# Optimization experiments

Hardware: AMD Instinct MI355X
Metric: run time of the kernel (lower is better)

The kernel has to match this reference:

```python
import jax, jax.numpy as jnp
import numpy as np
import math

D_IN, D_MODEL, D_STATE, STAGES, N_CLS = 2048, 64, 128, 20, 202
PHASE_MAX = math.pi / 50


def _layer_norm(x, g, b, eps=1e-5):
    mu = jnp.mean(x, axis=-1, keepdims=True)
    var = jnp.mean((x - mu) ** 2, axis=-1, keepdims=True)
    return (x - mu) * jax.lax.rsqrt(var + eps) * g + b


def _lru_scan(z, nu_log, theta_log, gamma_log, B_re, B_im, C_re, C_im, Dskip):
    # z: (B,T,D_MODEL). Diagonal complex linear recurrence h_t = lam*h_{t-1} + gamma*(B z_t).
    lam = jnp.exp(-jnp.exp(nu_log) + 1j * jnp.exp(theta_log))          # (N,) complex, |lam|<1
    gamma = jnp.exp(gamma_log)                                          # (N,)
    u = (jnp.einsum('btd,nd->btn', z, B_re)
         + 1j * jnp.einsum('btd,nd->btn', z, B_im)) * gamma             # (B,T,N) complex
    lam_bc = jnp.broadcast_to(lam, u.shape)

    def binop(a, b):
        la, ua = a
        lb, ub = b
        return la * lb, lb * ua + ub

    _, h = jax.lax.associative_scan(binop, (lam_bc, u), axis=1)         # (B,T,N) complex
    y = (jnp.einsum('btn,dn->btd', h.real, C_re)
         - jnp.einsum('btn,dn->btd', h.imag, C_im))                     # Re(C h)
    return y + Dskip * z


def setup_inputs() -> dict:
    key = jax.random.key(0)
    ks = jax.random.split(key, 16)
    x = jax.random.normal(ks[0], (8, 2048, D_IN), dtype=jnp.float32)

    ln0_g = jnp.ones((D_IN,), jnp.float32)
    ln0_b = jnp.zeros((D_IN,), jnp.float32)
    W_embed = jax.random.normal(ks[1], (D_IN, D_MODEL), jnp.float32) / np.sqrt(D_IN)
    b_embed = jnp.zeros((D_MODEL,), jnp.float32)

    # per-stage LRU params, stacked over STAGES
    r = jax.random.uniform(ks[2], (STAGES, D_STATE), minval=0.9, maxval=0.999)
    theta = jax.random.uniform(ks[3], (STAGES, D_STATE), minval=1e-4, maxval=PHASE_MAX)
    nu_log = jnp.log(-jnp.log(r))
    theta_log = jnp.log(theta)
    gamma_log = 0.5 * jnp.log(1.0 - r ** 2)
    B_re = jax.random.normal(ks[4], (STAGES, D_STATE, D_MODEL)) / np.sqrt(2 * D_MODEL)
    B_im = jax.random.normal(ks[5], (STAGES, D_STATE, D_MODEL)) / np.sqrt(2 * D_MODEL)
    C_re = jax.random.normal(ks[6], (STAGES, D_MODEL, D_STATE)) / np.sqrt(D_STATE)
    C_im = jax.random.normal(ks[7], (STAGES, D_MODEL, D_STATE)) / np.sqrt(D_STATE)
    Dskip = jax.random.normal(ks[8], (STAGES, D_MODEL))
    ln_g = jnp.ones((STAGES, D_MODEL), jnp.float32)
    ln_b = jnp.zeros((STAGES, D_MODEL), jnp.float32)

    W_cls = jax.random.normal(ks[9], (D_MODEL, N_CLS), jnp.float32) / np.sqrt(D_MODEL)
    b_cls = jnp.zeros((N_CLS,), jnp.float32)

    return dict(x=x, ln0_g=ln0_g, ln0_b=ln0_b, W_embed=W_embed, b_embed=b_embed,
                ln_g=ln_g, ln_b=ln_b, nu_log=nu_log, theta_log=theta_log,
                gamma_log=gamma_log, B_re=B_re, B_im=B_im, C_re=C_re, C_im=C_im,
                Dskip=Dskip, W_cls=W_cls, b_cls=b_cls)


def reference(x, ln0_g, ln0_b, W_embed, b_embed, ln_g, ln_b, nu_log, theta_log,
              gamma_log, B_re, B_im, C_re, C_im, Dskip, W_cls, b_cls):
    # dropout is identity at inference
    h = _layer_norm(x, ln0_g, ln0_b)
    h = h @ W_embed + b_embed                                           # (B,T,64)
    for s in range(STAGES):
        z = _layer_norm(h, ln_g[s], ln_b[s])
        h = h + _lru_scan(z, nu_log[s], theta_log[s], gamma_log[s],
                          B_re[s], B_im[s], C_re[s], C_im[s], Dskip[s])
    out = h @ W_cls + b_cls                                             # (B,T,202)
    return out[None, ...]                                               # (1,B,T,202)
```

## Files before the change

### kernel.cpp

```cpp
#include <hip/hip_runtime.h>

typedef float f32x4 __attribute__((ext_vector_type(4)));
typedef __bf16 bf16x8 __attribute__((ext_vector_type(8)));

#define NSTAGE 20
#define TSEQ   2048
#define NST    128
#define NP2    256
#define NCLS   202
#define NCHUNK 32
#define CHTOK  64

static __device__ __forceinline__ unsigned short f2b(float f) {
  return __builtin_bit_cast(unsigned short, (__bf16)f);
}

__global__ void lru_convert_kernel(const float* __restrict__ Wemb,
                                   const float* __restrict__ Bre, const float* __restrict__ Bim,
                                   const float* __restrict__ Cre, const float* __restrict__ Cim,
                                   const float* __restrict__ Wcls,
                                   unsigned short* __restrict__ Wt,
                                   unsigned short* __restrict__ Bws,
                                   unsigned short* __restrict__ Cws,
                                   unsigned short* __restrict__ Wclst)
{
  const int NWT = 64 * 2048;
  const int NB  = NSTAGE * NP2 * 64;
  const int NC  = NSTAGE * 64 * NP2;
  const int NWC = 208 * 64;
  int idx = blockIdx.x * 256 + threadIdx.x;
  if (idx < NWT) {
    int d = idx >> 11, k = idx & 2047;
    Wt[idx] = f2b(Wemb[k * 64 + d]);
  } else if (idx < NWT + NB) {
    int r = idx - NWT;
    int s = r / (NP2 * 64); int r2 = r % (NP2 * 64);
    int np = r2 >> 6, k = r2 & 63;
    int n = np >> 1, p = np & 1;
    float v = p ? Bim[(s * NST + n) * 64 + k] : Bre[(s * NST + n) * 64 + k];
    Bws[r] = f2b(v);
  } else if (idx < NWT + NB + NC) {
    int r = idx - NWT - NB;
    int s = r / (64 * NP2); int r2 = r % (64 * NP2);
    int d = r2 >> 8, np = r2 & 255;
    int n = np >> 1, p = np & 1;
    float v = p ? -Cim[(s * 64 + d) * NST + n] : Cre[(s * 64 + d) * NST + n];
    Cws[r] = f2b(v);
  } else if (idx < NWT + NB + NC + NWC) {
    int r = idx - NWT - NB - NC;
    int cls = r >> 6, k = r & 63;
    Wclst[r] = (cls < NCLS) ? f2b(Wcls[k * NCLS + cls]) : (unsigned short)0;
  }
}

__launch_bounds__(256)
__global__ void lru_embed_kernel(const float* __restrict__ x,
                                 const float* __restrict__ g0,
                                 const float* __restrict__ b0,
                                 const unsigned short* __restrict__ Wt,
                                 const float* __restrict__ bemb,
                                 float* __restrict__ h0)
{
  __shared__ __align__(16) unsigned short zb[16][72];
  __shared__ float mu_s[16], rs_s[16];

  const int tid = threadIdx.x;
  const int b  = blockIdx.x >> 7;
  const int t0 = (blockIdx.x & 127) * 16;
  const int w = tid >> 6, lane = tid & 63;
  const int cl = lane & 15, q = lane >> 4;
  const int tg = tid >> 4, g = tid & 15;

  for (int i = 0; i < 4; ++i) {
    int t = w * 4 + i;
    const float* xp = x + ((size_t)(b * TSEQ + t0 + t)) * 2048;
    float sum = 0.f, sq = 0.f;
    #pragma unroll
    for (int j = 0; j < 32; ++j) {
      float v = xp[lane + 64 * j];
      sum += v; sq += v * v;
    }
    #pragma unroll
    for (int m = 1; m < 64; m <<= 1) {
      sum += __shfl_xor(sum, m); sq += __shfl_xor(sq, m);
    }
    if (lane == 0) {
      float mu = sum * (1.f / 2048.f);
      float var = sq * (1.f / 2048.f) - mu * mu;
      mu_s[t] = mu;
      rs_s[t] = rsqrtf(var + 1e-5f);
    }
  }
  __syncthreads();

  {
    const int g4 = g * 4;
    const float muT = mu_s[tg], rsT = rs_s[tg];
    f32x4 acc = {0.f, 0.f, 0.f, 0.f};
    for (int kc = 0; kc < 32; ++kc) {
      __syncthreads();
      {
        const float* xp = x + ((size_t)(b * TSEQ + t0 + tg)) * 2048 + kc * 64 + g4;
        float4 xv = *(const float4*)xp;
        float4 gv = *(const float4*)&g0[kc * 64 + g4];
        float4 bv = *(const float4*)&b0[kc * 64 + g4];
        float z0 = (xv.x - muT) * rsT * gv.x + bv.x;
        float z1 = (xv.y - muT) * rsT * gv.y + bv.y;
        float z2 = (xv.z - muT) * rsT * gv.z + bv.z;
        float z3 = (xv.w - muT) * rsT * gv.w + bv.w;
        *(unsigned*)&zb[tg][g4]     = (unsigned)f2b(z0) | ((unsigned)f2b(z1) << 16);
        *(unsigned*)&zb[tg][g4 + 2] = (unsigned)f2b(z2) | ((unsigned)f2b(z3) << 16);
      }
      __syncthreads();
      bf16x8 a0 = *(const bf16x8*)((const char*)&zb[0][0] + cl * 144 + q * 16);
      bf16x8 a1 = *(const bf16x8*)((const char*)&zb[0][0] + cl * 144 + 64 + q * 16);
      const unsigned short* wp = Wt + ((size_t)(w * 16 + cl)) * 2048 + kc * 64 + q * 8;
      bf16x8 w0 = *(const bf16x8*)wp;
      bf16x8 w1 = *(const bf16x8*)(wp + 32);
      acc = __builtin_amdgcn_mfma_f32_16x16x32_bf16(a0, w0, acc, 0, 0, 0);
      acc = __builtin_amdgcn_mfma_f32_16x16x32_bf16(a1, w1, acc, 0, 0, 0);
    }
    int d = w * 16 + cl;
    float be = bemb[d];
    #pragma unroll
    for (int r = 0; r < 4; ++r)
      h0[((size_t)(b * TSEQ + t0 + q * 4 + r)) * 64 + d] = acc[r] + be;
  }
}

__launch_bounds__(256)
__global__ void lru_carry0_kernel(const float* __restrict__ h0,
                                  const unsigned short* __restrict__ Bws,
                                  const float* __restrict__ lng,
                                  const float* __restrict__ lnb,
                                  const float* __restrict__ nulog,
                                  const float* __restrict__ thlog,
                                  const float* __restrict__ gmlog,
                                  float* __restrict__ carr)
{
  __shared__ __align__(16) unsigned short zb[16][72];
  __shared__ __align__(16) float ucat[16][264];

  const int tid = threadIdx.x;
  const int b = blockIdx.x >> 5;
  const int c = blockIdx.x & 31;
  const int t0 = c * CHTOK;
  const int w = tid >> 6, lane = tid & 63;
  const int cl = lane & 15, q = lane >> 4;
  const int tg = tid >> 4, g = tid & 15;

  float lamr = 0.f, lami = 0.f, hr = 0.f, hi = 0.f;
  if (tid < NST) {
    float mag = __expf(-__expf(nulog[tid]));
    float th  = __expf(thlog[tid]);
    lamr = mag * __cosf(th);
    lami = mag * __sinf(th);
  }

  for (int sb = 0; sb < 4; ++sb) {
    int tb = t0 + sb * 16;
    __syncthreads();
    {
      float4 hv = *(const float4*)&h0[((size_t)(b * TSEQ + tb + tg)) * 64 + g * 4];
      float sum = hv.x + hv.y + hv.z + hv.w;
      sum += __shfl_xor(sum, 1); sum += __shfl_xor(sum, 2);
      sum += __shfl_xor(sum, 4); sum += __shfl_xor(sum, 8);
      float mu = sum * (1.f / 64.f);
      float d0 = hv.x - mu, d1 = hv.y - mu, d2 = hv.z - mu, d3 = hv.w - mu;
      float sq = d0 * d0 + d1 * d1 + d2 * d2 + d3 * d3;
      sq += __shfl_xor(sq, 1); sq += __shfl_xor(sq, 2);
      sq += __shfl_xor(sq, 4); sq += __shfl_xor(sq, 8);
      float rs = rsqrtf(sq * (1.f / 64.f) + 1e-5f);
      float4 gv = *(const float4*)&lng[g * 4];
      float4 bv = *(const float4*)&lnb[g * 4];
      float z0 = d0 * rs * gv.x + bv.x;
      float z1 = d1 * rs * gv.y + bv.y;
      float z2 = d2 * rs * gv.z + bv.z;
      float z3 = d3 * rs * gv.w + bv.w;
      *(unsigned*)&zb[tg][g * 4]     = (unsigned)f2b(z0) | ((unsigned)f2b(z1) << 16);
      *(unsigned*)&zb[tg][g * 4 + 2] = (unsigned)f2b(z2) | ((unsigned)f2b(z3) << 16);
    }
    __syncthreads();
    {
      bf16x8 a0 = *(const bf16x8*)((const char*)&zb[0][0] + cl * 144 + q * 16);
      bf16x8 a1 = *(const bf16x8*)((const char*)&zb[0][0] + cl * 144 + 64 + q * 16);
      #pragma unroll
      for (int ti = 0; ti < 4; ++ti) {
        int np0 = (w * 4 + ti) * 16;
        const unsigned short* bp = Bws + (np0 + cl) * 64 + q * 8;
        bf16x8 b0 = *(const bf16x8*)bp;
        bf16x8 b1 = *(const bf16x8*)(bp + 32);
        f32x4 acc = {0.f, 0.f, 0.f, 0.f};
        acc = __builtin_amdgcn_mfma_f32_16x16x32_bf16(a0, b0, acc, 0, 0, 0);
        acc = __builtin_amdgcn_mfma_f32_16x16x32_bf16(a1, b1, acc, 0, 0, 0);
        int np = np0 + cl;
        float gam = __expf(gmlog[np >> 1]);
        ucat[q * 4 + 0][np] = acc[0] * gam;
        ucat[q * 4 + 1][np] = acc[1] * gam;
        ucat[q * 4 + 2][np] = acc[2] * gam;
        ucat[q * 4 + 3][np] = acc[3] * gam;
      }
    }
    __syncthreads();
    if (tid < NST) {
      int n = tid;
      #pragma unroll
      for (int t = 0; t < 16; ++t) {
        float ur = ucat[t][2 * n], ui = ucat[t][2 * n + 1];
        float nr = fmaf(lamr, hr, fmaf(-lami, hi, ur));
        float ni = fmaf(lamr, hi, fmaf(lami, hr, ui));
        hr = nr; hi = ni;
      }
    }
  }
  if (tid < NST) {
    float* cw = carr + ((size_t)(b * NCHUNK + c)) * 256 + 2 * tid;
    cw[0] = hr;
    cw[1] = hi;
  }
}

__launch_bounds__(256)
__global__ void lru_applycarry_kernel(float* __restrict__ h0,
                                      const float* __restrict__ carrin,
                                      float* __restrict__ carrout,
                                      const unsigned short* __restrict__ Bws,
                                      const unsigned short* __restrict__ Cws,
                                      const float* __restrict__ lng,
                                      const float* __restrict__ lnb,
                                      const float* __restrict__ nulog,
                                      const float* __restrict__ thlog,
                                      const float* __restrict__ gmlog,
                                      const float* __restrict__ dskip,
                                      int s, int last,
                                      const unsigned short* __restrict__ Wclst,
                                      const float* __restrict__ bcls,
                                      float* __restrict__ out)
{
  __shared__ float hsm64[64][68];
  __shared__ float hs[16][68];
  __shared__ float zsm[16][68];
  __shared__ __align__(16) unsigned short zb[16][72];
  __shared__ __align__(16) float ucat[16][264];
  __shared__ __align__(16) unsigned short hcb[16][264];

  const int tid = threadIdx.x;
  const int b = blockIdx.x >> 5;
  const int c = blockIdx.x & 31;
  const int t0 = c * CHTOK;
  const int w = tid >> 6, lane = tid & 63;
  const int cl = lane & 15, q = lane >> 4;
  const int tg = tid >> 4, g = tid & 15;

  float lamr = 0.f, lami = 0.f, Pr = 0.f, Pi = 0.f;
  if (tid < NST) {
    int n = tid;
    float mag = __expf(-__expf(nulog[s * NST + n]));
    float th  = __expf(thlog[s * NST + n]);
    lamr = mag * __cosf(th);
    lami = mag * __sinf(th);
    float ar = lamr, ai = lami;
    #pragma unroll
    for (int it = 0; it < 6; ++it) {
      float nr = ar * ar - ai * ai;
      float ni = 2.f * ar * ai;
      ar = nr; ai = ni;
    }
    const float* cb = carrin + (size_t)b * NCHUNK * 256 + 2 * n;
    #pragma unroll 4
    for (int j = 0; j < c; ++j) {
      float cr = cb[j * 256];
      float ci = cb[j * 256 + 1];
      float nr = fmaf(ar, Pr, fmaf(-ai, Pi, cr));
      float ni = fmaf(ar, Pi, fmaf(ai, Pr, ci));
      Pr = nr; Pi = ni;
    }
  }

  float hr = Pr, hi = Pi;
  for (int sb = 0; sb < 4; ++sb) {
    int tb = t0 + sb * 16;
    __syncthreads();
    {
      float4 hv = *(const float4*)&h0[((size_t)(b * TSEQ + tb + tg)) * 64 + g * 4];
      hs[tg][g * 4 + 0] = hv.x; hs[tg][g * 4 + 1] = hv.y;
      hs[tg][g * 4 + 2] = hv.z; hs[tg][g * 4 + 3] = hv.w;
      float sum = hv.x + hv.y + hv.z + hv.w;
      sum += __shfl_xor(sum, 1); sum += __shfl_xor(sum, 2);
      sum += __shfl_xor(sum, 4); sum += __shfl_xor(sum, 8);
      float mu = sum * (1.f / 64.f);
      float d0 = hv.x - mu, d1 = hv.y - mu, d2 = hv.z - mu, d3 = hv.w - mu;
      float sq = d0 * d0 + d1 * d1 + d2 * d2 + d3 * d3;
      sq += __shfl_xor(sq, 1); sq += __shfl_xor(sq, 2);
      sq += __shfl_xor(sq, 4); sq += __shfl_xor(sq, 8);
      float rs = rsqrtf(sq * (1.f / 64.f) + 1e-5f);
      float4 gv = *(const float4*)&lng[s * 64 + g * 4];
      float4 bv = *(const float4*)&lnb[s * 64 + g * 4];
      float z0 = d0 * rs * gv.x + bv.x;
      float z1 = d1 * rs * gv.y + bv.y;
      float z2 = d2 * rs * gv.z + bv.z;
      float z3 = d3 * rs * gv.w + bv.w;
      zsm[tg][g * 4 + 0] = z0; zsm[tg][g * 4 + 1] = z1;
      zsm[tg][g * 4 + 2] = z2; zsm[tg][g * 4 + 3] = z3;
      *(unsigned*)&zb[tg][g * 4]     = (unsigned)f2b(z0) | ((unsigned)f2b(z1) << 16);
      *(unsigned*)&zb[tg][g * 4 + 2] = (unsigned)f2b(z2) | ((unsigned)f2b(z3) << 16);
    }
    __syncthreads();
    {
      bf16x8 a0 = *(const bf16x8*)((const char*)&zb[0][0] + cl * 144 + q * 16);
      bf16x8 a1 = *(const bf16x8*)((const char*)&zb[0][0] + cl * 144 + 64 + q * 16);
      const unsigned short* bb = Bws + (size_t)s * NP2 * 64;
      #pragma unroll
      for (int ti = 0; ti < 4; ++ti) {
        int np0 = (w * 4 + ti) * 16;
        const unsigned short* bp = bb + (np0 + cl) * 64 + q * 8;
        bf16x8 b0 = *(const bf16x8*)bp;
        bf16x8 b1 = *(const bf16x8*)(bp + 32);
        f32x4 acc = {0.f, 0.f, 0.f, 0.f};
        acc = __builtin_amdgcn_mfma_f32_16x16x32_bf16(a0, b0, acc, 0, 0, 0);
        acc = __builtin_amdgcn_mfma_f32_16x16x32_bf16(a1, b1, acc, 0, 0, 0);
        int np = np0 + cl;
        float gam = __expf(gmlog[s * NST + (np >> 1)]);
        ucat[q * 4 + 0][np] = acc[0] * gam;
        ucat[q * 4 + 1][np] = acc[1] * gam;
        ucat[q * 4 + 2][np] = acc[2] * gam;
        ucat[q * 4 + 3][np] = acc[3] * gam;
      }
    }
    __syncthreads();
    if (tid < NST) {
      int n = tid;
      #pragma unroll
      for (int t = 0; t < 16; ++t) {
        float ur = ucat[t][2 * n], ui = ucat[t][2 * n + 1];
        float nr = fmaf(lamr, hr, fmaf(-lami, hi, ur));
        float ni = fmaf(lamr, hi, fmaf(lami, hr, ui));
        hr = nr; hi = ni;
        *(unsigned*)&hcb[t][2 * n] = (unsigned)f2b(hr) | ((unsigned)f2b(hi) << 16);
      }
    }
    __syncthreads();
    {
      int d0 = w * 16;
      const unsigned short* cp = Cws + ((size_t)s * 64 + d0 + cl) * NP2 + q * 8;
      f32x4 acc = {0.f, 0.f, 0.f, 0.f};
      #pragma unroll
      for (int ks = 0; ks < 8; ++ks) {
        bf16x8 a  = *(const bf16x8*)((const char*)&hcb[0][0] + cl * 528 + ks * 64 + q * 16);
        bf16x8 cc = *(const bf16x8*)(cp + ks * 32);
        acc = __builtin_amdgcn_mfma_f32_16x16x32_bf16(a, cc, acc, 0, 0, 0);
      }
      int d = d0 + cl;
      float dk = dskip[s * 64 + d];
      #pragma unroll
      for (int r = 0; r < 4; ++r) {
        int t = q * 4 + r;
        hsm64[sb * 16 + t][d] = hs[t][d] + acc[r] + dk * zsm[t][d];
      }
    }
  }

  if (!last) {
    const int s1 = s + 1;
    float lam2r = 0.f, lam2i = 0.f, h2r = 0.f, h2i = 0.f;
    if (tid < NST) {
      float mag = __expf(-__expf(nulog[s1 * NST + tid]));
      float th  = __expf(thlog[s1 * NST + tid]);
      lam2r = mag * __cosf(th);
      lam2i = mag * __sinf(th);
    }
    for (int sb = 0; sb < 4; ++sb) {
      __syncthreads();
      {
        float4 hv = *(const float4*)&hsm64[sb * 16 + tg][g * 4];
        float sum = hv.x + hv.y + hv.z + hv.w;
        sum += __shfl_xor(sum, 1); sum += __shfl_xor(sum, 2);
        sum += __shfl_xor(sum, 4); sum += __shfl_xor(sum, 8);
        float mu = sum * (1.f / 64.f);
        float d0 = hv.x - mu, d1 = hv.y - mu, d2 = hv.z - mu, d3 = hv.w - mu;
        float sq = d0 * d0 + d1 * d1 + d2 * d2 + d3 * d3;
        sq += __shfl_xor(sq, 1); sq += __shfl_xor(sq, 2);
        sq += __shfl_xor(sq, 4); sq += __shfl_xor(sq, 8);
        float rs = rsqrtf(sq * (1.f / 64.f) + 1e-5f);
        float4 gv = *(const float4*)&lng[s1 * 64 + g * 4];
        float4 bv = *(const float4*)&lnb[s1 * 64 + g * 4];
        float z0 = d0 * rs * gv.x + bv.x;
        float z1 = d1 * rs * gv.y + bv.y;
        float z2 = d2 * rs * gv.z + bv.z;
        float z3 = d3 * rs * gv.w + bv.w;
        *(unsigned*)&zb[tg][g * 4]     = (unsigned)f2b(z0) | ((unsigned)f2b(z1) << 16);
        *(unsigned*)&zb[tg][g * 4 + 2] = (unsigned)f2b(z2) | ((unsigned)f2b(z3) << 16);
      }
      __syncthreads();
      {
        bf16x8 a0 = *(const bf16x8*)((const char*)&zb[0][0] + cl * 144 + q * 16);
        bf16x8 a1 = *(const bf16x8*)((const char*)&zb[0][0] + cl * 144 + 64 + q * 16);
        const unsigned short* bb = Bws + (size_t)s1 * NP2 * 64;
        #pragma unroll
        for (int ti = 0; ti < 4; ++ti) {
          int np0 = (w * 4 + ti) * 16;
          const unsigned short* bp = bb + (np0 + cl) * 64 + q * 8;
          bf16x8 b0 = *(const bf16x8*)bp;
          bf16x8 b1 = *(const bf16x8*)(bp + 32);
          f32x4 acc = {0.f, 0.f, 0.f, 0.f};
          acc = __builtin_amdgcn_mfma_f32_16x16x32_bf16(a0, b0, acc, 0, 0, 0);
          acc = __builtin_amdgcn_mfma_f32_16x16x32_bf16(a1, b1, acc, 0, 0, 0);
          int np = np0 + cl;
          float gam = __expf(gmlog[s1 * NST + (np >> 1)]);
          ucat[q * 4 + 0][np] = acc[0] * gam;
          ucat[q * 4 + 1][np] = acc[1] * gam;
          ucat[q * 4 + 2][np] = acc[2] * gam;
          ucat[q * 4 + 3][np] = acc[3] * gam;
        }
      }
      __syncthreads();
      if (tid < NST) {
        int n = tid;
        #pragma unroll
        for (int t = 0; t < 16; ++t) {
          float ur = ucat[t][2 * n], ui = ucat[t][2 * n + 1];
          float nr = fmaf(lam2r, h2r, fmaf(-lam2i, h2i, ur));
          float ni = fmaf(lam2r, h2i, fmaf(lam2i, h2r, ui));
          h2r = nr; h2i = ni;
        }
      }
    }
    if (tid < NST) {
      float* cw = carrout + ((size_t)(b * NCHUNK + c)) * 256 + 2 * tid;
      cw[0] = h2r;
      cw[1] = h2i;
    }
    #pragma unroll
    for (int sb = 0; sb < 4; ++sb) {
      float4 hv;
      hv.x = hsm64[sb * 16 + tg][g * 4 + 0];
      hv.y = hsm64[sb * 16 + tg][g * 4 + 1];
      hv.z = hsm64[sb * 16 + tg][g * 4 + 2];
      hv.w = hsm64[sb * 16 + tg][g * 4 + 3];
      *(float4*)&h0[((size_t)(b * TSEQ + t0 + sb * 16 + tg)) * 64 + g * 4] = hv;
    }
  } else {
    for (int sb = 0; sb < 4; ++sb) {
      int tb = t0 + sb * 16;
      __syncthreads();
      {
        *(unsigned*)&zb[tg][g * 4] =
            (unsigned)f2b(hsm64[sb * 16 + tg][g * 4 + 0]) |
            ((unsigned)f2b(hsm64[sb * 16 + tg][g * 4 + 1]) << 16);
        *(unsigned*)&zb[tg][g * 4 + 2] =
            (unsigned)f2b(hsm64[sb * 16 + tg][g * 4 + 2]) |
            ((unsigned)f2b(hsm64[sb * 16 + tg][g * 4 + 3]) << 16);
      }
      __syncthreads();
      bf16x8 a0 = *(const bf16x8*)((const char*)&zb[0][0] + cl * 144 + q * 16);
      bf16x8 a1 = *(const bf16x8*)((const char*)&zb[0][0] + cl * 144 + 64 + q * 16);
      for (int ti = w; ti < 13; ti += 4) {
        int cls0 = ti * 16;
        const unsigned short* wp = Wclst + (cls0 + cl) * 64 + q * 8;
        bf16x8 b0 = *(const bf16x8*)wp;
        bf16x8 b1 = *(const bf16x8*)(wp + 32);
        f32x4 acc = {0.f, 0.f, 0.f, 0.f};
        acc = __builtin_amdgcn_mfma_f32_16x16x32_bf16(a0, b0, acc, 0, 0, 0);
        acc = __builtin_amdgcn_mfma_f32_16x16x32_bf16(a1, b1, acc, 0, 0, 0);
        int cls = cls0 + cl;
        if (cls < NCLS) {
          float bc = bcls[cls];
          #pragma unroll
          for (int r = 0; r < 4; ++r) {
            int t = q * 4 + r;
            out[((size_t)(b * TSEQ + tb + t)) * NCLS + cls] = acc[r] + bc;
          }
        }
      }
    }
  }
}

extern "C" void kernel_launch(void* const* d_in, const int* in_sizes, int n_in,
                              void* d_out, int out_size, void* d_ws, size_t ws_size,
                              hipStream_t stream) {
  (void)in_sizes; (void)n_in; (void)out_size; (void)ws_size;
  const float* x     = (const float*)d_in[0];
  const float* ln0g  = (const float*)d_in[1];
  const float* ln0b  = (const float*)d_in[2];
  const float* Wemb  = (const float*)d_in[3];
  const float* bemb  = (const float*)d_in[4];
  const float* lng   = (const float*)d_in[5];
  const float* lnb   = (const float*)d_in[6];
  const float* nulog = (const float*)d_in[7];
  const float* thlog = (const float*)d_in[8];
  const float* gmlog = (const float*)d_in[9];
  const float* Bre   = (const float*)d_in[10];
  const float* Bim   = (const float*)d_in[11];
  const float* Cre   = (const float*)d_in[12];
  const float* Cim   = (const float*)d_in[13];
  const float* dskip = (const float*)d_in[14];
  const float* Wcls  = (const float*)d_in[15];
  const float* bcls  = (const float*)d_in[16];
  float* out = (float*)d_out;

  char* ws = (char*)d_ws;
  float* carrA         = (float*)(ws + 0);
  float* carrB         = (float*)(ws + 262144);
  unsigned short* Bws  = (unsigned short*)(ws + 524288);
  unsigned short* Cws  = (unsigned short*)(ws + 1179648);
  unsigned short* Wt   = (unsigned short*)(ws + 1835008);
  unsigned short* Wcl  = (unsigned short*)(ws + 2097152);
  float* h0            = (float*)(ws + 2123776);

  lru_convert_kernel<<<3124, 256, 0, stream>>>(Wemb, Bre, Bim, Cre, Cim, Wcls,
                                               Wt, Bws, Cws, Wcl);
  lru_embed_kernel<<<1024, 256, 0, stream>>>(x, ln0g, ln0b, Wt, bemb, h0);
  lru_carry0_kernel<<<256, 256, 0, stream>>>(h0, Bws, lng, lnb,
                                             nulog, thlog, gmlog, carrA);
  for (int s = 0; s < NSTAGE; ++s) {
    float* cin  = (s & 1) ? carrB : carrA;
    float* cout = (s & 1) ? carrA : carrB;
    lru_applycarry_kernel<<<256, 256, 0, stream>>>(h0, cin, cout, Bws, Cws,
                                                   lng, lnb, nulog, thlog,
                                                   gmlog, dskip, s,
                                                   (s == NSTAGE - 1) ? 1 : 0,
                                                   Wcl, bcls, out);
  }
}
```

Measured before the change: 661.2 us.

## Shrink scan chunks to 16 tokens, fuse carry0 into embed, drop LDS staging

The chunked scan now uses 128 chunks of 16 tokens per batch instead of 32 chunks of 64. Each stage kernel therefore launches 1024 blocks rather than 256 and processes a single 16-token tile with no inner sub-block loop. The first-stage carry computation is fused into the embed kernel, removing one launch and a reread of h0. The embed GEMM now builds MFMA operands directly in registers, dropping the shared-memory staging and barriers. The cost is a longer serial carry-prefix loop per block (up to 127 carries instead of 31) and a four-times larger carry buffer.

Measured after the change: 856.7 us. 1.3x slower.

```diff
diff --git a/kernel.cpp b/kernel.cpp
--- a/kernel.cpp
+++ b/kernel.cpp
@@ -8,8 +8,6 @@
 #define NST    128
 #define NP2    256
 #define NCLS   202
-#define NCHUNK 32
-#define CHTOK  64
 
 static __device__ __forceinline__ unsigned short f2b(float f) {
   return __builtin_bit_cast(unsigned short, (__bf16)f);
@@ -59,14 +57,24 @@
                                  const float* __restrict__ b0,
                                  const unsigned short* __restrict__ Wt,
                                  const float* __restrict__ bemb,
-                                 float* __restrict__ h0)
+                                 const unsigned short* __restrict__ Bws,
+                                 const float* __restrict__ lng,
+                                 const float* __restrict__ lnb,
+                                 const float* __restrict__ nulog,
+                                 const float* __restrict__ thlog,
+                                 const float* __restrict__ gmlog,
+                                 float* __restrict__ h0,
+                                 float* __restrict__ carr)
 {
+  __shared__ float mu_s[16], rs_s[16];
+  __shared__ float hs[16][68];
   __shared__ __align__(16) unsigned short zb[16][72];
-  __shared__ float mu_s[16], rs_s[16];
+  __shared__ __align__(16) float ucat[16][264];
 
   const int tid = threadIdx.x;
   const int b  = blockIdx.x >> 7;
-  const int t0 = (blockIdx.x & 127) * 16;
+  const int c  = blockIdx.x & 127;
+  const int t0 = c * 16;
   const int w = tid >> 6, lane = tid & 63;
   const int cl = lane & 15, q = lane >> 4;
   const int tg = tid >> 4, g = tid & 15;
@@ -94,127 +102,108 @@
   __syncthreads();
 
   {
-    const int g4 = g * 4;
-    const float muT = mu_s[tg], rsT = rs_s[tg];
+    const float muT = mu_s[cl], rsT = rs_s[cl];
+    const float* xrow = x + ((size_t)(b * TSEQ + t0 + cl)) * 2048;
+    const unsigned short* wrow = Wt + ((size_t)(w * 16 + cl)) * 2048;
     f32x4 acc = {0.f, 0.f, 0.f, 0.f};
     for (int kc = 0; kc < 32; ++kc) {
-      __syncthreads();
-      {
-        const float* xp = x + ((size_t)(b * TSEQ + t0 + tg)) * 2048 + kc * 64 + g4;
-        float4 xv = *(const float4*)xp;
-        float4 gv = *(const float4*)&g0[kc * 64 + g4];
-        float4 bv = *(const float4*)&b0[kc * 64 + g4];
-        float z0 = (xv.x - muT) * rsT * gv.x + bv.x;
-        float z1 = (xv.y - muT) * rsT * gv.y + bv.y;
-        float z2 = (xv.z - muT) * rsT * gv.z + bv.z;
-        float z3 = (xv.w - muT) * rsT * gv.w + bv.w;
-        *(unsigned*)&zb[tg][g4]     = (unsigned)f2b(z0) | ((unsigned)f2b(z1) << 16);
-        *(unsigned*)&zb[tg][g4 + 2] = (unsigned)f2b(z2) | ((unsigned)f2b(z3) << 16);
+      #pragma unroll
+      for (int ks = 0; ks < 2; ++ks) {
+        int ko = kc * 64 + ks * 32 + q * 8;
+        float4 xa = *(const float4*)&xrow[ko];
+        float4 xb = *(const float4*)&xrow[ko + 4];
+        float4 ga = *(const float4*)&g0[ko];
+        float4 gb = *(const float4*)&g0[ko + 4];
+        float4 ba = *(const float4*)&b0[ko];
+        float4 bb = *(const float4*)&b0[ko + 4];
+        float z0 = (xa.x - muT) * rsT * ga.x + ba.x;
+        float z1 = (xa.y - muT) * rsT * ga.y + ba.y;
+        float z2 = (xa.z - muT) * rsT * ga.z + ba.z;
+        float z3 = (xa.w - muT) * rsT * ga.w + ba.w;
+        float z4 = (xb.x - muT) * rsT * gb.x + bb.x;
+        float z5 = (xb.y - muT) * rsT * gb.y + bb.y;
+        float z6 = (xb.z - muT) * rsT * gb.z + bb.z;
+        float z7 = (xb.w - muT) * rsT * gb.w + bb.w;
+        uint4 u;
+        u.x = (unsigned)f2b(z0) | ((unsigned)f2b(z1) << 16);
+        u.y = (unsigned)f2b(z2) | ((unsigned)f2b(z3) << 16);
+        u.z = (unsigned)f2b(z4) | ((unsigned)f2b(z5) << 16);
+        u.w = (unsigned)f2b(z6) | ((unsigned)f2b(z7) << 16);
+        bf16x8 a = __builtin_bit_cast(bf16x8, u);
+        bf16x8 wv = *(const bf16x8*)&wrow[ko];
+        acc = __builtin_amdgcn_mfma_f32_16x16x32_bf16(a, wv, acc, 0, 0, 0);
       }
-      __syncthreads();
-      bf16x8 a0 = *(const bf16x8*)((const char*)&zb[0][0] + cl * 144 + q * 16);
-      bf16x8 a1 = *(const bf16x8*)((const char*)&zb[0][0] + cl * 144 + 64 + q * 16);
-      const unsigned short* wp = Wt + ((size_t)(w * 16 + cl)) * 2048 + kc * 64 + q * 8;
-      bf16x8 w0 = *(const bf16x8*)wp;
-      bf16x8 w1 = *(const bf16x8*)(wp + 32);
-      acc = __builtin_amdgcn_mfma_f32_16x16x32_bf16(a0, w0, acc, 0, 0, 0);
-      acc = __builtin_amdgcn_mfma_f32_16x16x32_bf16(a1, w1, acc, 0, 0, 0);
     }
     int d = w * 16 + cl;
     float be = bemb[d];
     #pragma unroll
-    for (int r = 0; r < 4; ++r)
-      h0[((size_t)(b * TSEQ + t0 + q * 4 + r)) * 64 + d] = acc[r] + be;
-  }
-}
-
-__launch_bounds__(256)
-__global__ void lru_carry0_kernel(const float* __restrict__ h0,
-                                  const unsigned short* __restrict__ Bws,
-                                  const float* __restrict__ lng,
-                                  const float* __restrict__ lnb,
-                                  const float* __restrict__ nulog,
-                                  const float* __restrict__ thlog,
-                                  const float* __restrict__ gmlog,
-                                  float* __restrict__ carr)
-{
-  __shared__ __align__(16) unsigned short zb[16][72];
-  __shared__ __align__(16) float ucat[16][264];
-
-  const int tid = threadIdx.x;
-  const int b = blockIdx.x >> 5;
-  const int c = blockIdx.x & 31;
-  const int t0 = c * CHTOK;
-  const int w = tid >> 6, lane = tid & 63;
-  const int cl = lane & 15, q = lane >> 4;
-  const int tg = tid >> 4, g = tid & 15;
-
-  float lamr = 0.f, lami = 0.f, hr = 0.f, hi = 0.f;
+    for (int r = 0; r < 4; ++r) {
+      float hv = acc[r] + be;
+      hs[q * 4 + r][d] = hv;
+      h0[((size_t)(b * TSEQ + t0 + q * 4 + r)) * 64 + d] = hv;
+    }
+  }
+  __syncthreads();
+
+  {
+    float4 hv = *(const float4*)&hs[tg][g * 4];
+    float sum = hv.x + hv.y + hv.z + hv.w;
+    sum += __shfl_xor(sum, 1); sum += __shfl_xor(sum, 2);
+    sum += __shfl_xor(sum, 4); sum += __shfl_xor(sum, 8);
+    float mu = sum * (1.f / 64.f);
+    float d0 = hv.x - mu, d1 = hv.y - mu, d2 = hv.z - mu, d3 = hv.w - mu;
+    float sq = d0 * d0 + d1 * d1 + d2 * d2 + d3 * d3;
+    sq += __shfl_xor(sq, 1); sq += __shfl_xor(sq, 2);
+    sq += __shfl_xor(sq, 4); sq += __shfl_xor(sq, 8);
+    float rs = rsqrtf(sq * (1.f / 64.f) + 1e-5f);
+    float4 gv = *(const float4*)&lng[g * 4];
+    float4 bv = *(const float4*)&lnb[g * 4];
+    float z0 = d0 * rs * gv.x + bv.x;
+    float z1 = d1 * rs * gv.y + bv.y;
+    float z2 = d2 * rs * gv.z + bv.z;
+    float z3 = d3 * rs * gv.w + bv.w;
+    *(unsigned*)&zb[tg][g * 4]     = (unsigned)f2b(z0) | ((unsigned)f2b(z1) << 16);
+    *(unsigned*)&zb[tg][g * 4 + 2] = (unsigned)f2b(z2) | ((unsigned)f2b(z3) << 16);
+  }
+  __syncthreads();
+
+  {
+    bf16x8 a0 = *(const bf16x8*)((const char*)&zb[0][0] + cl * 144 + q * 16);
+    bf16x8 a1 = *(const bf16x8*)((const char*)&zb[0][0] + cl * 144 + 64 + q * 16);
+    #pragma unroll
+    for (int ti = 0; ti < 4; ++ti) {
+      int np0 = (w * 4 + ti) * 16;
+      const unsigned short* bp = Bws + (np0 + cl) * 64 + q * 8;
+      bf16x8 b0v = *(const bf16x8*)bp;
+      bf16x8 b1v = *(const bf16x8*)(bp + 32);
+      f32x4 acc = {0.f, 0.f, 0.f, 0.f};
+      acc = __builtin_amdgcn_mfma_f32_16x16x32_bf16(a0, b0v, acc, 0, 0, 0);
+      acc = __builtin_amdgcn_mfma_f32_16x16x32_bf16(a1, b1v, acc, 0, 0, 0);
+      int np = np0 + cl;
+      float gam = __expf(gmlog[np >> 1]);
+      ucat[q * 4 + 0][np] = acc[0] * gam;
+      ucat[q * 4 + 1][np] = acc[1] * gam;
+      ucat[q * 4 + 2][np] = acc[2] * gam;
+      ucat[q * 4 + 3][np] = acc[3] * gam;
+    }
+  }
+  __syncthreads();
+
   if (tid < NST) {
-    float mag = __expf(-__expf(nulog[tid]));
-    float th  = __expf(thlog[tid]);
-    lamr = mag * __cosf(th);
-    lami = mag * __sinf(th);
-  }
-
-  for (int sb = 0; sb < 4; ++sb) {
-    int tb = t0 + sb * 16;
-    __syncthreads();
-    {
-      float4 hv = *(const float4*)&h0[((size_t)(b * TSEQ + tb + tg)) * 64 + g * 4];
-      float sum = hv.x + hv.y + hv.z + hv.w;
-      sum += __shfl_xor(sum, 1); sum += __shfl_xor(sum, 2);
-      sum += __shfl_xor(sum, 4); sum += __shfl_xor(sum, 8);
-      float mu = sum * (1.f / 64.f);
-      float d0 = hv.x - mu, d1 = hv.y - mu, d2 = hv.z - mu, d3 = hv.w - mu;
-      float sq = d0 * d0 + d1 * d1 + d2 * d2 + d3 * d3;
-      sq += __shfl_xor(sq, 1); sq += __shfl_xor(sq, 2);
-      sq += __shfl_xor(sq, 4); sq += __shfl_xor(sq, 8);
-      float rs = rsqrtf(sq * (1.f / 64.f) + 1e-5f);
-      float4 gv = *(const float4*)&lng[g * 4];
-      float4 bv = *(const float4*)&lnb[g * 4];
-      float z0 = d0 * rs * gv.x + bv.x;
-      float z1 = d1 * rs * gv.y + bv.y;
-      float z2 = d2 * rs * gv.z + bv.z;
-      float z3 = d3 * rs * gv.w + bv.w;
-      *(unsigned*)&zb[tg][g * 4]     = (unsigned)f2b(z0) | ((unsigned)f2b(z1) << 16);
-      *(unsigned*)&zb[tg][g * 4 + 2] = (unsigned)f2b(z2) | ((unsigned)f2b(z3) << 16);
-    }
-    __syncthreads();
-    {
-      bf16x8 a0 = *(const bf16x8*)((const char*)&zb[0][0] + cl * 144 + q * 16);
-      bf16x8 a1 = *(const bf16x8*)((const char*)&zb[0][0] + cl * 144 + 64 + q * 16);
-      #pragma unroll
-      for (int ti = 0; ti < 4; ++ti) {
-        int np0 = (w * 4 + ti) * 16;
-        const unsigned short* bp = Bws + (np0 + cl) * 64 + q * 8;
-        bf16x8 b0 = *(const bf16x8*)bp;
-        bf16x8 b1 = *(const bf16x8*)(bp + 32);
-        f32x4 acc = {0.f, 0.f, 0.f, 0.f};
-        acc = __builtin_amdgcn_mfma_f32_16x16x32_bf16(a0, b0, acc, 0, 0, 0);
-        acc = __builtin_amdgcn_mfma_f32_16x16x32_bf16(a1, b1, acc, 0, 0, 0);
-        int np = np0 + cl;
-        float gam = __expf(gmlog[np >> 1]);
-        ucat[q * 4 + 0][np] = acc[0] * gam;
-        ucat[q * 4 + 1][np] = acc[1] * gam;
-        ucat[q * 4 + 2][np] = acc[2] * gam;
-        ucat[q * 4 + 3][np] = acc[3] * gam;
-      }
-    }
-    __syncthreads();
-    if (tid < NST) {
-      int n = tid;
-      #pragma unroll
-      for (int t = 0; t < 16; ++t) {
-        float ur = ucat[t][2 * n], ui = ucat[t][2 * n + 1];
-        float nr = fmaf(lamr, hr, fmaf(-lami, hi, ur));
-        float ni = fmaf(lamr, hi, fmaf(lami, hr, ui));
-        hr = nr; hi = ni;
-      }
-    }
-  }
-  if (tid < NST) {
-    float* cw = carr + ((size_t)(b * NCHUNK + c)) * 256 + 2 * tid;
+    int n = tid;
+    float mag = __expf(-__expf(nulog[n]));
+    float th  = __expf(thlog[n]);
+    float lamr = mag * __cosf(th);
+    float lami = mag * __sinf(th);
+    float hr = 0.f, hi = 0.f;
+    #pragma unroll
+    for (int t = 0; t < 16; ++t) {
+      float ur = ucat[t][2 * n], ui = ucat[t][2 * n + 1];
+      float nr = fmaf(lamr, hr, fmaf(-lami, hi, ur));
+      float ni = fmaf(lamr, hi, fmaf(lami, hr, ui));
+      hr = nr; hi = ni;
+    }
+    float* cw = carr + ((size_t)(b * 128 + c)) * 256 + 2 * n;
     cw[0] = hr;
     cw[1] = hi;
   }
@@ -237,7 +226,6 @@
                                       const float* __restrict__ bcls,
                                       float* __restrict__ out)
 {
-  __shared__ float hsm64[64][68];
   __shared__ float hs[16][68];
   __shared__ float zsm[16][68];
   __shared__ __align__(16) unsigned short zb[16][72];
@@ -245,9 +233,9 @@
   __shared__ __align__(16) unsigned short hcb[16][264];
 
   const int tid = threadIdx.x;
-  const int b = blockIdx.x >> 5;
-  const int c = blockIdx.x & 31;
-  const int t0 = c * CHTOK;
+  const int b = blockIdx.x >> 7;
+  const int c = blockIdx.x & 127;
+  const int t0 = c * 16;
   const int w = tid >> 6, lane = tid & 63;
   const int cl = lane & 15, q = lane >> 4;
   const int tg = tid >> 4, g = tid & 15;
@@ -261,12 +249,12 @@
     lami = mag * __sinf(th);
     float ar = lamr, ai = lami;
     #pragma unroll
-    for (int it = 0; it < 6; ++it) {
+    for (int it = 0; it < 4; ++it) {
       float nr = ar * ar - ai * ai;
       float ni = 2.f * ar * ai;
       ar = nr; ai = ni;
     }
-    const float* cb = carrin + (size_t)b * NCHUNK * 256 + 2 * n;
+    const float* cb = carrin + (size_t)b * 128 * 256 + 2 * n;
     #pragma unroll 4
     for (int j = 0; j < c; ++j) {
       float cr = cb[j * 256];
@@ -277,14 +265,93 @@
     }
   }
 
-  float hr = Pr, hi = Pi;
-  for (int sb = 0; sb < 4; ++sb) {
-    int tb = t0 + sb * 16;
-    __syncthreads();
+  {
+    float4 hv = *(const float4*)&h0[((size_t)(b * TSEQ + t0 + tg)) * 64 + g * 4];
+    hs[tg][g * 4 + 0] = hv.x; hs[tg][g * 4 + 1] = hv.y;
+    hs[tg][g * 4 + 2] = hv.z; hs[tg][g * 4 + 3] = hv.w;
+    float sum = hv.x + hv.y + hv.z + hv.w;
+    sum += __shfl_xor(sum, 1); sum += __shfl_xor(sum, 2);
+    sum += __shfl_xor(sum, 4); sum += __shfl_xor(sum, 8);
+    float mu = sum * (1.f / 64.f);
+    float d0 = hv.x - mu, d1 = hv.y - mu, d2 = hv.z - mu, d3 = hv.w - mu;
+    float sq = d0 * d0 + d1 * d1 + d2 * d2 + d3 * d3;
+    sq += __shfl_xor(sq, 1); sq += __shfl_xor(sq, 2);
+    sq += __shfl_xor(sq, 4); sq += __shfl_xor(sq, 8);
+    float rs = rsqrtf(sq * (1.f / 64.f) + 1e-5f);
+    float4 gv = *(const float4*)&lng[s * 64 + g * 4];
+    float4 bv = *(const float4*)&lnb[s * 64 + g * 4];
+    float z0 = d0 * rs * gv.x + bv.x;
+    float z1 = d1 * rs * gv.y + bv.y;
+    float z2 = d2 * rs * gv.z + bv.z;
+    float z3 = d3 * rs * gv.w + bv.w;
+    zsm[tg][g * 4 + 0] = z0; zsm[tg][g * 4 + 1] = z1;
+    zsm[tg][g * 4 + 2] = z2; zsm[tg][g * 4 + 3] = z3;
+    *(unsigned*)&zb[tg][g * 4]     = (unsigned)f2b(z0) | ((unsigned)f2b(z1) << 16);
+    *(unsigned*)&zb[tg][g * 4 + 2] = (unsigned)f2b(z2) | ((unsigned)f2b(z3) << 16);
+  }
+  __syncthreads();
+
+  {
+    bf16x8 a0 = *(const bf16x8*)((const char*)&zb[0][0] + cl * 144 + q * 16);
+    bf16x8 a1 = *(const bf16x8*)((const char*)&zb[0][0] + cl * 144 + 64 + q * 16);
+    const unsigned short* bb = Bws + (size_t)s * NP2 * 64;
+    #pragma unroll
+    for (int ti = 0; ti < 4; ++ti) {
+      int np0 = (w * 4 + ti) * 16;
+      const unsigned short* bp = bb + (np0 + cl) * 64 + q * 8;
+      bf16x8 b0v = *(const bf16x8*)bp;
+      bf16x8 b1v = *(const bf16x8*)(bp + 32);
+      f32x4 acc = {0.f, 0.f, 0.f, 0.f};
+      acc = __builtin_amdgcn_mfma_f32_16x16x32_bf16(a0, b0v, acc, 0, 0, 0);
+      acc = __builtin_amdgcn_mfma_f32_16x16x32_bf16(a1, b1v, acc, 0, 0, 0);
+      int np = np0 + cl;
+      float gam = __expf(gmlog[s * NST + (np >> 1)]);
+      ucat[q * 4 + 0][np] = acc[0] * gam;
+      ucat[q * 4 + 1][np] = acc[1] * gam;
+      ucat[q * 4 + 2][np] = acc[2] * gam;
+      ucat[q * 4 + 3][np] = acc[3] * gam;
+    }
+  }
+  __syncthreads();
+
+  if (tid < NST) {
+    int n = tid;
+    float hr = Pr, hi = Pi;
+    #pragma unroll
+    for (int t = 0; t < 16; ++t) {
+      float ur = ucat[t][2 * n], ui = ucat[t][2 * n + 1];
+      float nr = fmaf(lamr, hr, fmaf(-lami, hi, ur));
+      float ni = fmaf(lamr, hi, fmaf(lami, hr, ui));
+      hr = nr; hi = ni;
+      *(unsigned*)&hcb[t][2 * n] = (unsigned)f2b(hr) | ((unsigned)f2b(hi) << 16);
+    }
+  }
+  __syncthreads();
+
+  {
+    int d0 = w * 16;
+    const unsigned short* cp = Cws + ((size_t)s * 64 + d0 + cl) * NP2 + q * 8;
+    f32x4 acc = {0.f, 0.f, 0.f, 0.f};
+    #pragma unroll
+    for (int ks = 0; ks < 8; ++ks) {
+      bf16x8 a  = *(const bf16x8*)((const char*)&hcb[0][0] + cl * 528 + ks * 64 + q * 16);
+      bf16x8 cc = *(const bf16x8*)(cp + ks * 32);
+      acc = __builtin_amdgcn_mfma_f32_16x16x32_bf16(a, cc, acc, 0, 0, 0);
+    }
+    int d = d0 + cl;
+    float dk = dskip[s * 64 + d];
+    #pragma unroll
+    for (int r = 0; r < 4; ++r) {
+      int t = q * 4 + r;
+      hs[t][d] = hs[t][d] + acc[r] + dk * zsm[t][d];
+    }
+  }
+  __syncthreads();
+
+  if (!last) {
+    const int s1 = s + 1;
     {
-      float4 hv = *(const float4*)&h0[((size_t)(b * TSEQ + tb + tg)) * 64 + g * 4];
-      hs[tg][g * 4 + 0] = hv.x; hs[tg][g * 4 + 1] = hv.y;
-      hs[tg][g * 4 + 2] = hv.z; hs[tg][g * 4 + 3] = hv.w;
+      float4 hv = *(const float4*)&hs[tg][g * 4];
       float sum = hv.x + hv.y + hv.z + hv.w;
       sum += __shfl_xor(sum, 1); sum += __shfl_xor(sum, 2);
       sum += __shfl_xor(sum, 4); sum += __shfl_xor(sum, 8);
@@ -294,14 +361,12 @@
       sq += __shfl_xor(sq, 1); sq += __shfl_xor(sq, 2);
       sq += __shfl_xor(sq, 4); sq += __shfl_xor(sq, 8);
       float rs = rsqrtf(sq * (1.f / 64.f) + 1e-5f);
-      float4 gv = *(const float4*)&lng[s * 64 + g * 4];
-      float4 bv = *(const float4*)&lnb[s * 64 + g * 4];
+      float4 gv = *(const float4*)&lng[s1 * 64 + g * 4];
+      float4 bv = *(const float4*)&lnb[s1 * 64 + g * 4];
       float z0 = d0 * rs * gv.x + bv.x;
       float z1 = d1 * rs * gv.y + bv.y;
       float z2 = d2 * rs * gv.z + bv.z;
       float z3 = d3 * rs * gv.w + bv.w;
-      zsm[tg][g * 4 + 0] = z0; zsm[tg][g * 4 + 1] = z1;
-      zsm[tg][g * 4 + 2] = z2; zsm[tg][g * 4 + 3] = z3;
       *(unsigned*)&zb[tg][g * 4]     = (unsigned)f2b(z0) | ((unsigned)f2b(z1) << 16);
       *(unsigned*)&zb[tg][g * 4 + 2] = (unsigned)f2b(z2) | ((unsigned)f2b(z3) << 16);
     }
@@ -309,18 +374,18 @@
     {
       bf16x8 a0 = *(const bf16x8*)((const char*)&zb[0][0] + cl * 144 + q * 16);
       bf16x8 a1 = *(const bf16x8*)((const char*)&zb[0][0] + cl * 144 + 64 + q * 16);
-      const unsigned short* bb = Bws + (size_t)s * NP2 * 64;
+      const unsigned short* bb = Bws + (size_t)s1 * NP2 * 64;
       #pragma unroll
       for (int ti = 0; ti < 4; ++ti) {
         int np0 = (w * 4 + ti) * 16;
         const unsigned short* bp = bb + (np0 + cl) * 64 + q * 8;
-        bf16x8 b0 = *(const bf16x8*)bp;
-        bf16x8 b1 = *(const bf16x8*)(bp + 32);
+        bf16x8 b0v = *(const bf16x8*)bp;
+        bf16x8 b1v = *(const bf16x8*)(bp + 32);
         f32x4 acc = {0.f, 0.f, 0.f, 0.f};
-        acc = __builtin_amdgcn_mfma_f32_16x16x32_bf16(a0, b0, acc, 0, 0, 0);
-        acc = __builtin_amdgcn_mfma_f32_16x16x32_bf16(a1, b1, acc, 0, 0, 0);
+        acc = __builtin_amdgcn_mfma_f32_16x16x32_bf16(a0, b0v, acc, 0, 0, 0);
+        acc = __builtin_amdgcn_mfma_f32_16x16x32_bf16(a1, b1v, acc, 0, 0, 0);
         int np = np0 + cl;
-        float gam = __expf(gmlog[s * NST + (np >> 1)]);
+        float gam = __expf(gmlog[s1 * NST + (np >> 1)]);
         ucat[q * 4 + 0][np] = acc[0] * gam;
         ucat[q * 4 + 1][np] = acc[1] * gam;
         ucat[q * 4 + 2][np] = acc[2] * gam;
@@ -330,146 +395,53 @@
     __syncthreads();
     if (tid < NST) {
       int n = tid;
+      float mag = __expf(-__expf(nulog[s1 * NST + n]));
+      float th  = __expf(thlog[s1 * NST + n]);
+      float l2r = mag * __cosf(th);
+      float l2i = mag * __sinf(th);
+      float hr = 0.f, hi = 0.f;
       #pragma unroll
       for (int t = 0; t < 16; ++t) {
         float ur = ucat[t][2 * n], ui = ucat[t][2 * n + 1];
-        float nr = fmaf(lamr, hr, fmaf(-lami, hi, ur));
-        float ni = fmaf(lamr, hi, fmaf(lami, hr, ui));
+        float nr = fmaf(l2r, hr, fmaf(-l2i, hi, ur));
+        float ni = fmaf(l2r, hi, fmaf(l2i, hr, ui));
         hr = nr; hi = ni;
-        *(unsigned*)&hcb[t][2 * n] = (unsigned)f2b(hr) | ((unsigned)f2b(hi) << 16);
       }
+      float* cw = carrout + ((size_t)(b * 128 + c)) * 256 + 2 * n;
+      cw[0] = hr;
+      cw[1] = hi;
+    }
+    {
+      float4 hv;
+      hv.x = hs[tg][g * 4 + 0]; hv.y = hs[tg][g * 4 + 1];
+      hv.z = hs[tg][g * 4 + 2]; hv.w = hs[tg][g * 4 + 3];
+      *(float4*)&h0[((size_t)(b * TSEQ + t0 + tg)) * 64 + g * 4] = hv;
+    }
+  } else {
+    {
+      *(unsigned*)&zb[tg][g * 4] =
+          (unsigned)f2b(hs[tg][g * 4 + 0]) | ((unsigned)f2b(hs[tg][g * 4 + 1]) << 16);
+      *(unsigned*)&zb[tg][g * 4 + 2] =
+          (unsigned)f2b(hs[tg][g * 4 + 2]) | ((unsigned)f2b(hs[tg][g * 4 + 3]) << 16);
     }
     __syncthreads();
-    {
-      int d0 = w * 16;
-      const unsigned short* cp = Cws + ((size_t)s * 64 + d0 + cl) * NP2 + q * 8;
+    bf16x8 a0 = *(const bf16x8*)((const char*)&zb[0][0] + cl * 144 + q * 16);
+    bf16x8 a1 = *(const bf16x8*)((const char*)&zb[0][0] + cl * 144 + 64 + q * 16);
+    for (int ti = w; ti < 13; ti += 4) {
+      int cls0 = ti * 16;
+      const unsigned short* wp = Wclst + (cls0 + cl) * 64 + q * 8;
+      bf16x8 b0v = *(const bf16x8*)wp;
+      bf16x8 b1v = *(const bf16x8*)(wp + 32);
       f32x4 acc = {0.f, 0.f, 0.f, 0.f};
-      #pragma unroll
-      for (int ks = 0; ks < 8; ++ks) {
-        bf16x8 a  = *(const bf16x8*)((const char*)&hcb[0][0] + cl * 528 + ks * 64 + q * 16);
-        bf16x8 cc = *(const bf16x8*)(cp + ks * 32);
-        acc = __builtin_amdgcn_mfma_f32_16x16x32_bf16(a, cc, acc, 0, 0, 0);
-      }
-      int d = d0 + cl;
-      float dk = dskip[s * 64 + d];
-      #pragma unroll
-      for (int r = 0; r < 4; ++r) {
-        int t = q * 4 + r;
-        hsm64[sb * 16 + t][d] = hs[t][d] + acc[r] + dk * zsm[t][d];
-      }
-    }
-  }
-
-  if (!last) {
-    const int s1 = s + 1;
-    float lam2r = 0.f, lam2i = 0.f, h2r = 0.f, h2i = 0.f;
-    if (tid < NST) {
-      float mag = __expf(-__expf(nulog[s1 * NST + tid]));
-      float th  = __expf(thlog[s1 * NST + tid]);
-      lam2r = mag * __cosf(th);
-      lam2i = mag * __sinf(th);
-    }
-    for (int sb = 0; sb < 4; ++sb) {
-      __syncthreads();
-      {
-        float4 hv = *(const float4*)&hsm64[sb * 16 + tg][g * 4];
-        float sum = hv.x + hv.y + hv.z + hv.w;
-        sum += __shfl_xor(sum, 1); sum += __shfl_xor(sum, 2);
-        sum += __shfl_xor(sum, 4); sum += __shfl_xor(sum, 8);
-        float mu = sum * (1.f / 64.f);
-        float d0 = hv.x - mu, d1 = hv.y - mu, d2 = hv.z - mu, d3 = hv.w - mu;
-        float sq = d0 * d0 + d1 * d1 + d2 * d2 + d3 * d3;
-        sq += __shfl_xor(sq, 1); sq += __shfl_xor(sq, 2);
-        sq += __shfl_xor(sq, 4); sq += __shfl_xor(sq, 8);
-        float rs = rsqrtf(sq * (1.f / 64.f) + 1e-5f);
-        float4 gv = *(const float4*)&lng[s1 * 64 + g * 4];
-        float4 bv = *(const float4*)&lnb[s1 * 64 + g * 4];
-        float z0 = d0 * rs * gv.x + bv.x;
-        float z1 = d1 * rs * gv.y + bv.y;
-        float z2 = d2 * rs * gv.z + bv.z;
-        float z3 = d3 * rs * gv.w + bv.w;
-        *(unsigned*)&zb[tg][g * 4]     = (unsigned)f2b(z0) | ((unsigned)f2b(z1) << 16);
-        *(unsigned*)&zb[tg][g * 4 + 2] = (unsigned)f2b(z2) | ((unsigned)f2b(z3) << 16);
-      }
-      __syncthreads();
-      {
-        bf16x8 a0 = *(const bf16x8*)((const char*)&zb[0][0] + cl * 144 + q * 16);
-        bf16x8 a1 = *(const bf16x8*)((const char*)&zb[0][0] + cl * 144 + 64 + q * 16);
-        const unsigned short* bb = Bws + (size_t)s1 * NP2 * 64;
+      acc = __builtin_amdgcn_mfma_f32_16x16x32_bf16(a0, b0v, acc, 0, 0, 0);
+      acc = __builtin_amdgcn_mfma_f32_16x16x32_bf16(a1, b1v, acc, 0, 0, 0);
+      int cls = cls0 + cl;
+      if (cls < NCLS) {
+        float bc = bcls[cls];
         #pragma unroll
-        for (int ti = 0; ti < 4; ++ti) {
-          int np0 = (w * 4 + ti) * 16;
-          const unsigned short* bp = bb + (np0 + cl) * 64 + q * 8;
-          bf16x8 b0 = *(const bf16x8*)bp;
-          bf16x8 b1 = *(const bf16x8*)(bp + 32);
-          f32x4 acc = {0.f, 0.f, 0.f, 0.f};
-          acc = __builtin_amdgcn_mfma_f32_16x16x32_bf16(a0, b0, acc, 0, 0, 0);
-          acc = __builtin_amdgcn_mfma_f32_16x16x32_bf16(a1, b1, acc, 0, 0, 0);
-          int np = np0 + cl;
-          float gam = __expf(gmlog[s1 * NST + (np >> 1)]);
-          ucat[q * 4 + 0][np] = acc[0] * gam;
-          ucat[q * 4 + 1][np] = acc[1] * gam;
-          ucat[q * 4 + 2][np] = acc[2] * gam;
-          ucat[q * 4 + 3][np] = acc[3] * gam;
-        }
-      }
-      __syncthreads();
-      if (tid < NST) {
-        int n = tid;
-        #pragma unroll
-        for (int t = 0; t < 16; ++t) {
-          float ur = ucat[t][2 * n], ui = ucat[t][2 * n + 1];
-          float nr = fmaf(lam2r, h2r, fmaf(-lam2i, h2i, ur));
-          float ni = fmaf(lam2r, h2i, fmaf(lam2i, h2r, ui));
-          h2r = nr; h2i = ni;
-        }
-      }
-    }
-    if (tid < NST) {
-      float* cw = carrout + ((size_t)(b * NCHUNK + c)) * 256 + 2 * tid;
-      cw[0] = h2r;
-      cw[1] = h2i;
-    }
-    #pragma unroll
-    for (int sb = 0; sb < 4; ++sb) {
-      float4 hv;
-      hv.x = hsm64[sb * 16 + tg][g * 4 + 0];
-      hv.y = hsm64[sb * 16 + tg][g * 4 + 1];
-      hv.z = hsm64[sb * 16 + tg][g * 4 + 2];
-      hv.w = hsm64[sb * 16 + tg][g * 4 + 3];
-      *(float4*)&h0[((size_t)(b * TSEQ + t0 + sb * 16 + tg)) * 64 + g * 4] = hv;
-    }
-  } else {
-    for (int sb = 0; sb < 4; ++sb) {
-      int tb = t0 + sb * 16;
-      __syncthreads();
-      {
-        *(unsigned*)&zb[tg][g * 4] =
-            (unsigned)f2b(hsm64[sb * 16 + tg][g * 4 + 0]) |
-            ((unsigned)f2b(hsm64[sb * 16 + tg][g * 4 + 1]) << 16);
-        *(unsigned*)&zb[tg][g * 4 + 2] =
-            (unsigned)f2b(hsm64[sb * 16 + tg][g * 4 + 2]) |
-            ((unsigned)f2b(hsm64[sb * 16 + tg][g * 4 + 3]) << 16);
-      }
-      __syncthreads();
-      bf16x8 a0 = *(const bf16x8*)((const char*)&zb[0][0] + cl * 144 + q * 16);
-      bf16x8 a1 = *(const bf16x8*)((const char*)&zb[0][0] + cl * 144 + 64 + q * 16);
-      for (int ti = w; ti < 13; ti += 4) {
-        int cls0 = ti * 16;
-        const unsigned short* wp = Wclst + (cls0 + cl) * 64 + q * 8;
-        bf16x8 b0 = *(const bf16x8*)wp;
-        bf16x8 b1 = *(const bf16x8*)(wp + 32);
-        f32x4 acc = {0.f, 0.f, 0.f, 0.f};
-        acc = __builtin_amdgcn_mfma_f32_16x16x32_bf16(a0, b0, acc, 0, 0, 0);
-        acc = __builtin_amdgcn_mfma_f32_16x16x32_bf16(a1, b1, acc, 0, 0, 0);
-        int cls = cls0 + cl;
-        if (cls < NCLS) {
-          float bc = bcls[cls];
-          #pragma unroll
-          for (int r = 0; r < 4; ++r) {
-            int t = q * 4 + r;
-            out[((size_t)(b * TSEQ + tb + t)) * NCLS + cls] = acc[r] + bc;
-          }
+        for (int r = 0; r < 4; ++r) {
+          int t = q * 4 + r;
+          out[((size_t)(b * TSEQ + t0 + t)) * NCLS + cls] = acc[r] + bc;
         }
       }
     }
@@ -501,25 +473,25 @@
 
   char* ws = (char*)d_ws;
   float* carrA         = (float*)(ws + 0);
-  float* carrB         = (float*)(ws + 262144);
-  unsigned short* Bws  = (unsigned short*)(ws + 524288);
-  unsigned short* Cws  = (unsigned short*)(ws + 1179648);
-  unsigned short* Wt   = (unsigned short*)(ws + 1835008);
-  unsigned short* Wcl  = (unsigned short*)(ws + 2097152);
-  float* h0            = (float*)(ws + 2123776);
+  float* carrB         = (float*)(ws + 1048576);
+  unsigned short* Bws  = (unsigned short*)(ws + 2097152);
+  unsigned short* Cws  = (unsigned short*)(ws + 2752512);
+  unsigned short* Wt   = (unsigned short*)(ws + 3407872);
+  unsigned short* Wcl  = (unsigned short*)(ws + 3670016);
+  float* h0            = (float*)(ws + 3696640);
 
   lru_convert_kernel<<<3124, 256, 0, stream>>>(Wemb, Bre, Bim, Cre, Cim, Wcls,
                                                Wt, Bws, Cws, Wcl);
-  lru_embed_kernel<<<1024, 256, 0, stream>>>(x, ln0g, ln0b, Wt, bemb, h0);
-  lru_carry0_kernel<<<256, 256, 0, stream>>>(h0, Bws, lng, lnb,
-                                             nulog, thlog, gmlog, carrA);
+  lru_embed_kernel<<<1024, 256, 0, stream>>>(x, ln0g, ln0b, Wt, bemb, Bws,
+                                             lng, lnb, nulog, thlog, gmlog,
+                                             h0, carrA);
   for (int s = 0; s < NSTAGE; ++s) {
     float* cin  = (s & 1) ? carrB : carrA;
     float* cout = (s & 1) ? carrA : carrB;
-    lru_applycarry_kernel<<<256, 256, 0, stream>>>(h0, cin, cout, Bws, Cws,
-                                                   lng, lnb, nulog, thlog,
-                                                   gmlog, dskip, s,
-                                                   (s == NSTAGE - 1) ? 1 : 0,
-                                                   Wcl, bcls, out);
+    lru_applycarry_kernel<<<1024, 256, 0, stream>>>(h0, cin, cout, Bws, Cws,
+                                                    lng, lnb, nulog, thlog,
+                                                    gmlog, dskip, s,
+                                                    (s == NSTAGE - 1) ? 1 : 0,
+                                                    Wcl, bcls, out);
   }
 }
```
